# Kernel tuning notes

Hardware: AMD Instinct MI355X
Metric: run time of the kernel (lower is better)

The kernel has to match this reference:

```python
import jax, jax.numpy as jnp
import numpy as np

B, S, D = 2, 2048, 1024
H, KVH, HD = 16, 4, 64          # query heads, kv heads, head dim
E, TOPK, F = 8, 2, 4096          # experts, top-k, expert intermediate
BAL_COEF = 0.01
EPS = 1e-6
ROPE_THETA = 10000.0


def setup_inputs() -> dict:
    key = jax.random.key(0)
    ks = jax.random.split(key, 10)
    g = lambda k, shape, sc=0.02: jax.random.normal(k, shape, dtype=jnp.float32) * sc
    return {
        "hidden_states": jax.random.normal(ks[0], (B, S, D), dtype=jnp.float32),
        "ln1_w": jnp.ones((D,), jnp.float32),
        "wq": g(ks[1], (D, H * HD)),
        "wk": g(ks[2], (D, KVH * HD)),
        "wv": g(ks[3], (D, KVH * HD)),
        "wo": g(ks[4], (H * HD, D)),
        "ln2_w": jnp.ones((D,), jnp.float32),
        "router_w": g(ks[5], (E, D)),
        "w_gate": g(ks[6], (E, D, F)),
        "w_up": g(ks[7], (E, D, F)),
        "w_down": g(ks[8], (E, F, D)),
    }


def rmsnorm(x, w):
    var = jnp.mean(jnp.square(x), axis=-1, keepdims=True)
    return x * jax.lax.rsqrt(var + EPS) * w


def apply_rope(x, pos):
    # x: [B, S, h, d]; HF rotate-half convention
    d = x.shape[-1]
    inv_freq = 1.0 / (ROPE_THETA ** (jnp.arange(0, d, 2, dtype=jnp.float32) / d))
    ang = pos.astype(jnp.float32)[:, None] * inv_freq[None, :]        # [S, d/2]
    cos = jnp.cos(ang)[None, :, None, :]
    sin = jnp.sin(ang)[None, :, None, :]
    x1, x2 = jnp.split(x, 2, axis=-1)
    return jnp.concatenate([x1 * cos - x2 * sin, x2 * cos + x1 * sin], axis=-1)


def reference(hidden_states, ln1_w, wq, wk, wv, wo, ln2_w, router_w, w_gate, w_up, w_down):
    b, s, d = hidden_states.shape
    pos = jnp.arange(s)

    # ---- RMSNorm -> GQA -> residual ----
    h = rmsnorm(hidden_states, ln1_w)
    q = (h @ wq).reshape(b, s, H, HD)
    k = (h @ wk).reshape(b, s, KVH, HD)
    v = (h @ wv).reshape(b, s, KVH, HD)
    q = apply_rope(q, pos)
    k = apply_rope(k, pos)
    rep = H // KVH
    k = jnp.repeat(k, rep, axis=2)   # [B,S,H,HD]
    v = jnp.repeat(v, rep, axis=2)

    scores = jnp.einsum("bshd,bthd->bhst", q, k) * (HD ** -0.5)
    causal = jnp.tril(jnp.ones((s, s), dtype=bool))
    scores = jnp.where(causal[None, None], scores, jnp.finfo(scores.dtype).min)
    attn = jax.nn.softmax(scores, axis=-1)
    ctx = jnp.einsum("bhst,bthd->bshd", attn, v).reshape(b, s, H * HD)
    hidden_states = hidden_states + ctx @ wo

    # ---- RMSNorm -> MoE -> residual ----
    h2 = rmsnorm(hidden_states, ln2_w)
    x = h2.reshape(-1, d)                                    # [T, D]
    logits = x @ router_w.T                                  # [T, E]
    probs = jax.nn.softmax(logits, axis=-1)
    top_p, top_i = jax.lax.top_k(probs, TOPK)                # [T, K]
    top_p = top_p / jnp.sum(top_p, axis=-1, keepdims=True)   # renormalize
    gates = jnp.zeros_like(probs).at[jnp.arange(x.shape[0])[:, None], top_i].set(top_p)  # [T, E]

    moe_out = jnp.zeros_like(x)
    for e in range(E):  # fixed small expert count
        gate = jax.nn.silu(x @ w_gate[e]) * (x @ w_up[e])    # SwiGLU [T, F]
        moe_out = moe_out + gates[:, e:e + 1] * (gate @ w_down[e])

    # ---- load-balancing aux loss (Switch-style) ----
    sel = jnp.sum(jax.nn.one_hot(top_i, E, dtype=probs.dtype), axis=1)  # [T, E]
    frac = jnp.mean(sel, axis=0) / TOPK                       # fraction routed, sums to 1
    prob_mean = jnp.mean(probs, axis=0)
    balance_loss = BAL_COEF * E * jnp.sum(frac * prob_mean)

    out = hidden_states + moe_out.reshape(b, s, d)
    return out, balance_loss
```

## Files before the change

kernel.cpp:

```cpp
#include <hip/hip_runtime.h>

#define Tt 4096
#define Bb 2
#define Ss 2048
#define Dd 1024
#define Hh 16
#define KVHn 4
#define HDn 64
#define En 8
#define Fn 4096

#define BM 128
#define BN 128

typedef unsigned short u16;
typedef __attribute__((ext_vector_type(4))) float f32x4;
typedef __attribute__((ext_vector_type(8))) short bfrag;
typedef __attribute__((ext_vector_type(4))) short s16x4;

#define WAITV(N) asm volatile("s_waitcnt vmcnt(" #N ")" ::: "memory")
#define BARRIER() asm volatile("s_barrier" ::: "memory")

__device__ __forceinline__ u16 f2bf(float f) {
    unsigned u = __builtin_bit_cast(unsigned, f);
    u = (u + 0x7fffu + ((u >> 16) & 1u)) >> 16;
    return (u16)u;
}
__device__ __forceinline__ float bf2f(u16 b) {
    unsigned u = ((unsigned)b) << 16;
    return __builtin_bit_cast(float, u);
}
__device__ __forceinline__ void split8a(const float* va, bfrag* ph, bfrag* pl) {
    bfrag th, tl;
#pragma unroll
    for (int j = 0; j < 8; j++) {
        u16 hu = f2bf(va[j]);
        th[j] = (short)hu;
        tl[j] = (short)f2bf(va[j] - bf2f(hu));
    }
    *ph = th; *pl = tl;
}
__device__ __forceinline__ void glds16(const void* g, void* l) {
    __builtin_amdgcn_global_load_lds(
        (const __attribute__((address_space(1))) unsigned int*)g,
        (__attribute__((address_space(3))) unsigned int*)l, 16, 0, 0);
}

template<bool SPL>
__global__ __launch_bounds__(256)
void tconv_k(const float* __restrict__ src, u16* __restrict__ dhi, u16* __restrict__ dlo,
             const int K, const int N, const int rowOff, const int nTilesN)
{
    const int tid = threadIdx.x;
    const int ty = blockIdx.x / nTilesN, tx = blockIdx.x % nTilesN;
    const int k0 = ty * 64, n0 = tx * 64;
    __shared__ float tl[64][65];
#pragma unroll
    for (int it = 0; it < 16; it++) {
        int idx = tid + it * 256;
        int kk = idx >> 6, nn = idx & 63;
        tl[kk][nn] = src[(size_t)(k0 + kk) * N + n0 + nn];
    }
    __syncthreads();
#pragma unroll
    for (int it = 0; it < 8; it++) {
        int idx = tid + it * 256;
        int n = idx >> 5, k2 = (idx & 31) * 2;
        float v0 = tl[k2][n], v1 = tl[k2 + 1][n];
        u16 h0 = f2bf(v0), h1v = f2bf(v1);
        size_t o = (size_t)(rowOff + n0 + n) * K + k0 + k2;
        *(unsigned*)&dhi[o] = (unsigned)h0 | ((unsigned)h1v << 16);
        if (SPL) {
            u16 l0 = f2bf(v0 - bf2f(h0)), l1 = f2bf(v1 - bf2f(h1v));
            *(unsigned*)&dlo[o] = (unsigned)l0 | ((unsigned)l1 << 16);
        }
    }
}

template<int TBK, bool SWZ>
__global__ __launch_bounds__(256)
void tprep_k(const float* __restrict__ src, u16* __restrict__ dst,
             const int K, const int N, const int nTilesN)
{
    const int tid = threadIdx.x;
    const int e = blockIdx.y;
    const int ntl = blockIdx.x % nTilesN, kt = blockIdx.x / nTilesN;
    const int nTK = K / TBK;
    src += (size_t)e * K * N + (size_t)(kt * TBK) * N + ntl * 128;
    u16* dblk = dst + (((size_t)e * nTilesN + ntl) * nTK + kt) * (size_t)(128 * TBK);
    __shared__ float tl[TBK][132];
#pragma unroll
    for (int it = 0; it < TBK / 8; it++) {
        int i4 = tid + it * 256;
        int kk = i4 >> 5, n = (i4 & 31) * 4;
        f32x4 v = *(const f32x4*)(src + (size_t)kk * N + n);
        tl[kk][n] = v.x; tl[kk][n + 1] = v.y; tl[kk][n + 2] = v.z; tl[kk][n + 3] = v.w;
    }
    __syncthreads();
#pragma unroll
    for (int it = 0; it < TBK / 16; it++) {
        int idx = tid + it * 256;
        int n = (TBK == 32) ? (idx >> 2) : (idx >> 3);
        int c = (TBK == 32) ? (idx & 3) : (idx & 7);
        bfrag v;
#pragma unroll
        for (int j = 0; j < 8; j++) v[j] = (short)f2bf(tl[c * 8 + j][n]);
        int boff = n * (TBK * 2) + ((c * 16) ^ (SWZ ? ((n & 7) << 4) : 0));
        *(bfrag*)((char*)dblk + boff) = v;
    }
}

__global__ __launch_bounds__(256)
void rmsnorm_split_k(const float* __restrict__ x, const float* __restrict__ w,
                     u16* __restrict__ ohi, u16* __restrict__ olo)
{
    const int row = blockIdx.x;
    const int tid = threadIdx.x;
    const int lane = tid & 63, wid = tid >> 6;
    f32x4 t4 = *(const f32x4*)(x + (size_t)row * Dd + tid * 4);
    float s = t4.x*t4.x + t4.y*t4.y + t4.z*t4.z + t4.w*t4.w;
#pragma unroll
    for (int o = 1; o < 64; o <<= 1) s += __shfl_xor(s, o, 64);
    __shared__ float red[4];
    if (lane == 0) red[wid] = s;
    __syncthreads();
    float inv = rsqrtf((red[0] + red[1] + red[2] + red[3]) * (1.0f / Dd) + 1e-6f);
    f32x4 w4 = *(const f32x4*)(w + tid * 4);
    float va[4] = { t4.x*inv*w4.x, t4.y*inv*w4.y, t4.z*inv*w4.z, t4.w*inv*w4.w };
    s16x4 hi, lo;
#pragma unroll
    for (int j = 0; j < 4; j++) {
        u16 hu = f2bf(va[j]);
        hi[j] = (short)hu;
        lo[j] = (short)f2bf(va[j] - bf2f(hu));
    }
    *(s16x4*)&ohi[(size_t)row * Dd + tid * 4] = hi;
    *(s16x4*)&olo[(size_t)row * Dd + tid * 4] = lo;
}

__global__ __launch_bounds__(256)
void rmsnorm2_k(const float* __restrict__ x, const float* __restrict__ w,
                float* __restrict__ of, u16* __restrict__ ob)
{
    const int row = blockIdx.x;
    const int tid = threadIdx.x;
    const int lane = tid & 63, wid = tid >> 6;
    f32x4 t4 = *(const f32x4*)(x + (size_t)row * Dd + tid * 4);
    float s = t4.x*t4.x + t4.y*t4.y + t4.z*t4.z + t4.w*t4.w;
#pragma unroll
    for (int o = 1; o < 64; o <<= 1) s += __shfl_xor(s, o, 64);
    __shared__ float red[4];
    if (lane == 0) red[wid] = s;
    __syncthreads();
    float inv = rsqrtf((red[0] + red[1] + red[2] + red[3]) * (1.0f / Dd) + 1e-6f);
    f32x4 w4 = *(const f32x4*)(w + tid * 4);
    f32x4 o4;
    o4.x = t4.x*inv*w4.x; o4.y = t4.y*inv*w4.y; o4.z = t4.z*inv*w4.z; o4.w = t4.w*inv*w4.w;
    *(f32x4*)&of[(size_t)row * Dd + tid * 4] = o4;
    s16x4 hb;
    hb[0] = (short)f2bf(o4.x); hb[1] = (short)f2bf(o4.y);
    hb[2] = (short)f2bf(o4.z); hb[3] = (short)f2bf(o4.w);
    *(s16x4*)&ob[(size_t)row * Dd + tid * 4] = hb;
}

__global__ __launch_bounds__(256)
void rope_tab_k(float* __restrict__ ct, float* __restrict__ st)
{
    int idx = blockIdx.x * 256 + threadIdx.x;
    if (idx < Ss * 32) {
        int s = idx >> 5, i = idx & 31;
        double inv = pow(10000.0, -((double)(2 * i)) / 64.0);
        double a = (double)s * inv;
        double sn, cs;
        sincos(a, &sn, &cs);
        ct[idx] = (float)cs;
        st[idx] = (float)sn;
    }
}

__global__ __launch_bounds__(256)
void rope_q_k(float* __restrict__ qkv, const float* __restrict__ ct, const float* __restrict__ st)
{
    int idx = blockIdx.x * 256 + threadIdx.x;
    int i = idx & 31, hh = (idx >> 5) & (Hh - 1), t = idx >> 9;
    int s = t & (Ss - 1);
    float cs = ct[s * 32 + i], sn = st[s * 32 + i];
    float* base = qkv + (size_t)t * 1536 + hh * 64 + i;
    float x1 = base[0], x2 = base[32];
    base[0]  = x1 * cs - x2 * sn;
    base[32] = x2 * cs + x1 * sn;
}

__global__ __launch_bounds__(256)
void kprep_k(const float* __restrict__ qkv, const float* __restrict__ ct,
             const float* __restrict__ st, u16* __restrict__ khi, u16* __restrict__ klo)
{
    int idx = blockIdx.x * 256 + threadIdx.x;
    int i = idx & 31, hh = (idx >> 5) & (KVHn - 1), t = idx >> 7;
    int s = t & (Ss - 1);
    float cs = ct[s * 32 + i], sn = st[s * 32 + i];
    const float* base = qkv + (size_t)t * 1536 + 1024 + hh * 64 + i;
    float x1 = base[0], x2 = base[32];
    float r1 = x1 * cs - x2 * sn, r2 = x2 * cs + x1 * sn;
    size_t o = (size_t)t * (KVHn * HDn) + hh * 64 + i;
    u16 h1v = f2bf(r1), h2v = f2bf(r2);
    khi[o] = h1v;       khi[o + 32] = h2v;
    klo[o] = f2bf(r1 - bf2f(h1v));
    klo[o + 32] = f2bf(r2 - bf2f(h2v));
}

__global__ __launch_bounds__(256)
void vprep_k(const float* __restrict__ qkv, u16* __restrict__ vthi, u16* __restrict__ vtlo)
{
    const int st0 = blockIdx.x * 64;
    const int g = blockIdx.y;
    const int b = g >> 2, kvh = g & 3;
    const int tid = threadIdx.x;
    __shared__ float tl[64][65];
#pragma unroll
    for (int it = 0; it < 16; it++) {
        int idx = tid + it * 256;
        int sl = idx >> 6, d = idx & 63;
        tl[sl][d] = qkv[(size_t)(b * Ss + st0 + sl) * 1536 + 1280 + kvh * 64 + d];
    }
    __syncthreads();
#pragma unroll
    for (int it = 0; it < 8; it++) {
        int idx = tid + it * 256;
        int d = idx >> 5, s2 = (idx & 31) * 2;
        float v0 = tl[s2][d], v1 = tl[s2 + 1][d];
        u16 h0 = f2bf(v0), h1v = f2bf(v1);
        size_t o = ((size_t)g * 64 + d) * Ss + st0 + s2;
        *(unsigned*)&vthi[o] = (unsigned)h0 | ((unsigned)h1v << 16);
        u16 l0 = f2bf(v0 - bf2f(h0)), l1 = f2bf(v1 - bf2f(h1v));
        *(unsigned*)&vtlo[o] = (unsigned)l0 | ((unsigned)l1 << 16);
    }
}

template<bool RESID>
__global__ __launch_bounds__(256)
void gemm_split_k(const u16* __restrict__ Ahi_g, const u16* __restrict__ Alo_g,
                  const u16* __restrict__ Bhi_g, const u16* __restrict__ Blo_g,
                  float* __restrict__ C, const float* __restrict__ resid,
                  const int M, const int N, const int K, const int ntiles)
{
    const int bid = blockIdx.x;
    const int nt = bid % ntiles, mt = bid / ntiles;
    __shared__ __align__(16) u16 Ah[2][128 * 32], Al[2][128 * 32];
    __shared__ __align__(16) u16 Bh[2][128 * 32], Bl[2][128 * 32];
    const int tid = threadIdx.x, lane = tid & 63, wid = tid >> 6;
    const int wrow = (wid >> 1) * 64, wcol = (wid & 1) * 64;
    const int l15 = lane & 15, lhi = lane >> 4;
    const int row0 = mt * BM, col0 = nt * BN;

    const u16 *ah_s[2], *al_s[2], *bh_s[2], *bl_s[2];
#pragma unroll
    for (int j = 0; j < 2; j++) {
        int r = (wid * 2 + j) * 16 + (lane >> 2);
        size_t ca = (size_t)(row0 + r) * K + (lane & 3) * 8;
        size_t cb = (size_t)(col0 + r) * K + (lane & 3) * 8;
        ah_s[j] = Ahi_g + ca; al_s[j] = Alo_g + ca;
        bh_s[j] = Bhi_g + cb; bl_s[j] = Blo_g + cb;
    }
    f32x4 acc[4][4];
#pragma unroll
    for (int i = 0; i < 4; i++)
#pragma unroll
        for (int j = 0; j < 4; j++) { acc[i][j].x = 0.f; acc[i][j].y = 0.f; acc[i][j].z = 0.f; acc[i][j].w = 0.f; }

    auto stage = [&](int buf, int k0) {
#pragma unroll
        for (int j = 0; j < 2; j++) {
            int d = (wid * 2 + j) * 512;
            glds16(ah_s[j] + k0, &Ah[buf][d]);
            glds16(al_s[j] + k0, &Al[buf][d]);
            glds16(bh_s[j] + k0, &Bh[buf][d]);
            glds16(bl_s[j] + k0, &Bl[buf][d]);
        }
    };
    auto compute = [&](int cur) {
        bfrag ah[4], al[4], bh[4], bl[4];
#pragma unroll
        for (int mi = 0; mi < 4; mi++) {
            int rb = (wrow + mi * 16 + l15) * 32 + lhi * 8;
            ah[mi] = *(const bfrag*)&Ah[cur][rb];
            al[mi] = *(const bfrag*)&Al[cur][rb];
        }
#pragma unroll
        for (int ni = 0; ni < 4; ni++) {
            int rb = (wcol + ni * 16 + l15) * 32 + lhi * 8;
            bh[ni] = *(const bfrag*)&Bh[cur][rb];
            bl[ni] = *(const bfrag*)&Bl[cur][rb];
        }
#pragma unroll
        for (int mi = 0; mi < 4; mi++)
#pragma unroll
            for (int ni = 0; ni < 4; ni++) {
                acc[mi][ni] = __builtin_amdgcn_mfma_f32_16x16x32_bf16(ah[mi], bh[ni], acc[mi][ni], 0, 0, 0);
                acc[mi][ni] = __builtin_amdgcn_mfma_f32_16x16x32_bf16(ah[mi], bl[ni], acc[mi][ni], 0, 0, 0);
                acc[mi][ni] = __builtin_amdgcn_mfma_f32_16x16x32_bf16(al[mi], bh[ni], acc[mi][ni], 0, 0, 0);
            }
    };
    const int nkt = K / 32;
    stage(0, 0);
    stage(1, 32);
    int cur = 0;
    for (int kt = 0; kt < nkt - 1; kt++) {
        WAITV(8);
        BARRIER();
        compute(cur);
        BARRIER();
        if (kt + 2 < nkt) stage(cur, (kt + 2) * 32);
        cur ^= 1;
    }
    WAITV(0);
    BARRIER();
    compute(cur);
#pragma unroll
    for (int mi = 0; mi < 4; mi++) {
#pragma unroll
        for (int t = 0; t < 4; t++) {
            int pr = row0 + wrow + mi * 16 + lhi * 4 + t;
#pragma unroll
            for (int ni = 0; ni < 4; ni++) {
                int gc = col0 + wcol + ni * 16 + l15;
                float vv = acc[mi][ni][t];
                if (RESID) vv += resid[(size_t)pr * N + gc];
                C[(size_t)pr * N + gc] = vv;
            }
        }
    }
}

template<int MODE>
__global__ __launch_bounds__(256, 4)
void gemm_expert_k(const u16* __restrict__ A_g, const u16* __restrict__ Bt,
                   u16* __restrict__ act,
                   const int* __restrict__ toklist, const float* __restrict__ gwlist,
                   const int* __restrict__ counts, const int* __restrict__ offsets)
{
    const int e = blockIdx.y;
    const int Meff = counts[e];
    const int nt = blockIdx.x & 31, mt = blockIdx.x >> 5;
    if (mt * BM >= Meff) return;
    const int* tok = toklist + e * Tt;
    const float* gw = gwlist + e * Tt;
    const int rowoff = offsets[e];
    __shared__ __align__(16) u16 As[2][128 * 32], Bs[2][128 * 32];
    const int tid = threadIdx.x, lane = tid & 63, wid = tid >> 6;
    const int wrow = (wid >> 1) * 64, wcol = (wid & 1) * 64;
    const int l15 = lane & 15, lhi = lane >> 4;
    const int row0 = mt * BM, col0 = nt * BN;

    const u16* asrc[2];
#pragma unroll
    for (int j = 0; j < 2; j++) {
        int row = (wid * 2 + j) * 16 + (lane >> 2);
        int pr = row0 + row;
        int tr = (pr < Meff) ? tok[pr] : tok[0];
        asrc[j] = A_g + (size_t)tr * Dd + (lane & 3) * 8;
    }
    const size_t bblk = (size_t)(e * 32 + nt) * (32 * 4096);
    const u16* bsrc = Bt + bblk + (size_t)(wid * 2) * 512 + lane * 8;

    f32x4 acc[4][4];
#pragma unroll
    for (int i = 0; i < 4; i++)
#pragma unroll
        for (int j = 0; j < 4; j++) { acc[i][j].x = 0.f; acc[i][j].y = 0.f; acc[i][j].z = 0.f; acc[i][j].w = 0.f; }

    auto stage = [&](int buf, int kt) {
#pragma unroll
        for (int j = 0; j < 2; j++) {
            int d = (wid * 2 + j) * 512;
            glds16(asrc[j] + kt * 32,                  &As[buf][d]);
            glds16(bsrc + j * 512 + (size_t)kt * 4096, &Bs[buf][d]);
        }
    };
    auto compute = [&](int cur) {
        bfrag a[4];
#pragma unroll
        for (int mi = 0; mi < 4; mi++)
            a[mi] = *(const bfrag*)&As[cur][(wrow + mi * 16 + l15) * 32 + lhi * 8];
#pragma unroll
        for (int ni = 0; ni < 4; ni++) {
            bfrag b = *(const bfrag*)&Bs[cur][(wcol + ni * 16 + l15) * 32 + lhi * 8];
#pragma unroll
            for (int mi = 0; mi < 4; mi++)
                acc[mi][ni] = __builtin_amdgcn_mfma_f32_16x16x32_bf16(a[mi], b, acc[mi][ni], 0, 0, 0);
        }
    };
    stage(0, 0);
    stage(1, 1);
    int cur = 0;
    for (int kt = 0; kt < 31; kt++) {
        WAITV(4);
        BARRIER();
        compute(cur);
        BARRIER();
        if (kt + 2 < 32) stage(cur, kt + 2);
        cur ^= 1;
    }
    WAITV(0);
    BARRIER();
    compute(cur);
#pragma unroll
    for (int mi = 0; mi < 4; mi++) {
#pragma unroll
        for (int t = 0; t < 4; t++) {
            int pr = row0 + wrow + mi * 16 + lhi * 4 + t;
            if (pr < Meff) {
                float gwv = (MODE == 1) ? gw[pr] : 0.f;
#pragma unroll
                for (int ni = 0; ni < 4; ni++) {
                    int gc = col0 + wcol + ni * 16 + l15;
                    size_t ix = (size_t)(rowoff + pr) * Fn + gc;
                    if (MODE == 0) {
                        act[ix] = f2bf(acc[mi][ni][t]);
                    } else {
                        float g = bf2f(act[ix]);
                        float sg = g / (1.0f + expf(-g));
                        act[ix] = f2bf(sg * acc[mi][ni][t] * gwv);
                    }
                }
            }
        }
    }
}

__global__ __launch_bounds__(256, 4)
void gemm_down_k(const u16* __restrict__ act, const u16* __restrict__ Bt,
                 float* __restrict__ C, const int* __restrict__ toklist,
                 const int* __restrict__ counts, const int* __restrict__ offsets)
{
    const int e = blockIdx.y;
    const int Meff = counts[e];
    const int nt = blockIdx.x & 7, mt = blockIdx.x >> 3;
    if (mt * BM >= Meff) return;
    const int* tok = toklist + e * Tt;
    const int rowoff = offsets[e];
    __shared__ __align__(16) u16 As[2][128 * 32], Bs[2][128 * 32];
    const int tid = threadIdx.x, lane = tid & 63, wid = tid >> 6;
    const int wrow = (wid >> 1) * 64, wcol = (wid & 1) * 64;
    const int l15 = lane & 15, lhi = lane >> 4;
    const int row0 = mt * BM;

    const u16* asrc[2];
#pragma unroll
    for (int j = 0; j < 2; j++) {
        int row = (wid * 2 + j) * 16 + (lane >> 2);
        int pr = row0 + row;
        int rr = (pr < Meff) ? pr : 0;
        asrc[j] = act + (size_t)(rowoff + rr) * Fn + (lane & 3) * 8;
    }
    const size_t bblk = (size_t)(e * 8 + nt) * ((size_t)128 * 4096);
    const u16* bsrc = Bt + bblk + (size_t)(wid * 2) * 512 + lane * 8;

    f32x4 acc[4][4];
#pragma unroll
    for (int i = 0; i < 4; i++)
#pragma unroll
        for (int j = 0; j < 4; j++) { acc[i][j].x = 0.f; acc[i][j].y = 0.f; acc[i][j].z = 0.f; acc[i][j].w = 0.f; }

    auto stage = [&](int buf, int kt) {
#pragma unroll
        for (int j = 0; j < 2; j++) {
            int d = (wid * 2 + j) * 512;
            glds16(asrc[j] + kt * 32,                  &As[buf][d]);
            glds16(bsrc + j * 512 + (size_t)kt * 4096, &Bs[buf][d]);
        }
    };
    auto compute = [&](int cur) {
        bfrag a[4];
#pragma unroll
        for (int mi = 0; mi < 4; mi++)
            a[mi] = *(const bfrag*)&As[cur][(wrow + mi * 16 + l15) * 32 + lhi * 8];
#pragma unroll
        for (int ni = 0; ni < 4; ni++) {
            bfrag b = *(const bfrag*)&Bs[cur][(wcol + ni * 16 + l15) * 32 + lhi * 8];
#pragma unroll
            for (int mi = 0; mi < 4; mi++)
                acc[mi][ni] = __builtin_amdgcn_mfma_f32_16x16x32_bf16(a[mi], b, acc[mi][ni], 0, 0, 0);
        }
    };
    stage(0, 0);
    stage(1, 1);
    int cur = 0;
    const int nkt = Fn / 32;
    for (int kt = 0; kt < nkt - 1; kt++) {
        WAITV(4);
        BARRIER();
        compute(cur);
        BARRIER();
        if (kt + 2 < nkt) stage(cur, kt + 2);
        cur ^= 1;
    }
    WAITV(0);
    BARRIER();
    compute(cur);
#pragma unroll
    for (int mi = 0; mi < 4; mi++) {
#pragma unroll
        for (int t = 0; t < 4; t++) {
            int pr = row0 + wrow + mi * 16 + lhi * 4 + t;
            if (pr < Meff) {
                int trow = tok[pr];
#pragma unroll
                for (int ni = 0; ni < 4; ni++) {
                    int gc = nt * BN + wcol + ni * 16 + l15;
                    atomicAdd(&C[(size_t)trow * Dd + gc], acc[mi][ni][t]);
                }
            }
        }
    }
}

__global__ __launch_bounds__(256)
void attn_k(const float* __restrict__ qkv, const u16* __restrict__ khi,
            const u16* __restrict__ klo, const u16* __restrict__ vthi,
            const u16* __restrict__ vtlo, u16* __restrict__ chi, u16* __restrict__ clo)
{
    const int qt = (int)gridDim.x - 1 - (int)blockIdx.x;
    const int h = blockIdx.y, b = blockIdx.z;
    const int kvh = h >> 2;
    const int g = b * KVHn + kvh;
    const int tid = threadIdx.x;
    const int lane = tid & 63, wid = tid >> 6;
    const int l15 = lane & 15, lhi = lane >> 4;

    __shared__ __align__(16) u16 Khi[64 * 64];
    __shared__ __align__(16) u16 Klo[64 * 64];
    __shared__ __align__(16) u16 Vhi[64 * 72];
    __shared__ __align__(16) u16 Vlo[64 * 72];
    __shared__ __align__(16) u16 Phi[4 * 16 * 72];
    __shared__ __align__(16) u16 Plo[4 * 16 * 72];

    bfrag qh[2], ql[2];
    {
        const int qrow = qt * 64 + wid * 16 + l15;
        const float* qb = qkv + (size_t)(b * Ss + qrow) * 1536 + h * 64;
#pragma unroll
        for (int ks = 0; ks < 2; ks++) {
            const float* p = qb + ks * 32 + lhi * 8;
            f32x4 u0 = *(const f32x4*)p;
            f32x4 u1 = *(const f32x4*)(p + 4);
            float va[8] = { u0.x * 0.125f, u0.y * 0.125f, u0.z * 0.125f, u0.w * 0.125f,
                            u1.x * 0.125f, u1.y * 0.125f, u1.z * 0.125f, u1.w * 0.125f };
            split8a(va, &qh[ks], &ql[ks]);
        }
    }
    size_t kga[2], vga[2];
    int kboff[2], vboff[2];
#pragma unroll
    for (int it = 0; it < 2; it++) {
        int ci = tid + it * 256;
        int kv = ci >> 3, d0 = (ci & 7) << 3;
        kga[it] = (size_t)(b * Ss + kv) * (KVHn * HDn) + kvh * 64 + d0;
        kboff[it] = kv * 128 + ((d0 * 2) ^ ((kv & 7) << 4));
        int d = ci >> 3, kv0 = (ci & 7) << 3;
        vga[it] = ((size_t)g * 64 + d) * Ss + kv0;
        vboff[it] = d * 72 + kv0;
    }
    bfrag rkh[2], rkl[2], rvh[2], rvl[2];
    auto LOADR = [&](int kt) {
#pragma unroll
        for (int it = 0; it < 2; it++) {
            size_t ga = kga[it] + (size_t)kt * (64 * KVHn * HDn);
            rkh[it] = *(const bfrag*)&khi[ga];
            rkl[it] = *(const bfrag*)&klo[ga];
            size_t gv = vga[it] + (size_t)kt * 64;
            rvh[it] = *(const bfrag*)&vthi[gv];
            rvl[it] = *(const bfrag*)&vtlo[gv];
        }
    };
    f32x4 O[4];
#pragma unroll
    for (int ni = 0; ni < 4; ni++) { O[ni].x = 0.f; O[ni].y = 0.f; O[ni].z = 0.f; O[ni].w = 0.f; }
    float m_s = -1e30f;
    float l_s = 0.f;

    LOADR(0);
    for (int kt = 0; kt <= qt; kt++) {
#pragma unroll
        for (int it = 0; it < 2; it++) {
            *(bfrag*)((char*)Khi + kboff[it]) = rkh[it];
            *(bfrag*)((char*)Klo + kboff[it]) = rkl[it];
            *(bfrag*)&Vhi[vboff[it]] = rvh[it];
            *(bfrag*)&Vlo[vboff[it]] = rvl[it];
        }
        __syncthreads();
        if (kt < qt) LOADR(kt + 1);
        f32x4 sf[4];
#pragma unroll
        for (int ni = 0; ni < 4; ni++) { sf[ni].x = 0.f; sf[ni].y = 0.f; sf[ni].z = 0.f; sf[ni].w = 0.f; }
        __builtin_amdgcn_s_setprio(1);
#pragma unroll
        for (int ks = 0; ks < 2; ks++) {
#pragma unroll
            for (int ni = 0; ni < 4; ni++) {
                int kv = ni * 16 + l15;
                int dof = ks * 64 + lhi * 16;
                int boff = kv * 128 + (dof ^ ((kv & 7) << 4));
                bfrag kfh = *(const bfrag*)((const char*)Khi + boff);
                bfrag kfl = *(const bfrag*)((const char*)Klo + boff);
                sf[ni] = __builtin_amdgcn_mfma_f32_16x16x32_bf16(kfh, qh[ks], sf[ni], 0, 0, 0);
                sf[ni] = __builtin_amdgcn_mfma_f32_16x16x32_bf16(kfl, qh[ks], sf[ni], 0, 0, 0);
                sf[ni] = __builtin_amdgcn_mfma_f32_16x16x32_bf16(kfh, ql[ks], sf[ni], 0, 0, 0);
            }
        }
        __builtin_amdgcn_s_setprio(0);
        if (kt == qt) {
#pragma unroll
            for (int ni = 0; ni < 4; ni++)
#pragma unroll
                for (int t = 0; t < 4; t++)
                    if (ni * 16 + lhi * 4 + t > wid * 16 + l15) sf[ni][t] = -1e30f;
        }
        float mx = -1e30f;
#pragma unroll
        for (int ni = 0; ni < 4; ni++)
#pragma unroll
            for (int t = 0; t < 4; t++) mx = fmaxf(mx, sf[ni][t]);
        mx = fmaxf(mx, __shfl_xor(mx, 16, 64));
        mx = fmaxf(mx, __shfl_xor(mx, 32, 64));
        float mn = fmaxf(m_s, mx);
        float sc = expf(m_s - mn);
        m_s = mn;
        float rs = 0.f;
#pragma unroll
        for (int ni = 0; ni < 4; ni++)
#pragma unroll
            for (int t = 0; t < 4; t++) {
                float p = expf(sf[ni][t] - mn);
                sf[ni][t] = p;
                rs += p;
            }
        rs += __shfl_xor(rs, 16, 64);
        rs += __shfl_xor(rs, 32, 64);
        l_s = l_s * sc + rs;
#pragma unroll
        for (int ni = 0; ni < 4; ni++)
#pragma unroll
            for (int t = 0; t < 4; t++) O[ni][t] *= sc;
#pragma unroll
        for (int ni = 0; ni < 4; ni++)
#pragma unroll
            for (int t = 0; t < 4; t++) {
                float p = sf[ni][t];
                u16 hu = f2bf(p);
                int ix = (wid * 16 + l15) * 72 + ni * 16 + lhi * 4 + t;
                Phi[ix] = hu;
                Plo[ix] = f2bf(p - bf2f(hu));
            }
        asm volatile("s_waitcnt lgkmcnt(0)" ::: "memory");
        __builtin_amdgcn_sched_barrier(0);
        __builtin_amdgcn_s_setprio(1);
#pragma unroll
        for (int ks = 0; ks < 2; ks++) {
            int pb = (wid * 16 + l15) * 72 + ks * 32 + lhi * 8;
            bfrag pfh = *(const bfrag*)&Phi[pb];
            bfrag pfl = *(const bfrag*)&Plo[pb];
#pragma unroll
            for (int ni = 0; ni < 4; ni++) {
                int vb = (ni * 16 + l15) * 72 + ks * 32 + lhi * 8;
                bfrag vfh = *(const bfrag*)&Vhi[vb];
                bfrag vfl = *(const bfrag*)&Vlo[vb];
                O[ni] = __builtin_amdgcn_mfma_f32_16x16x32_bf16(vfh, pfh, O[ni], 0, 0, 0);
                O[ni] = __builtin_amdgcn_mfma_f32_16x16x32_bf16(vfl, pfh, O[ni], 0, 0, 0);
                O[ni] = __builtin_amdgcn_mfma_f32_16x16x32_bf16(vfh, pfl, O[ni], 0, 0, 0);
            }
        }
        __builtin_amdgcn_s_setprio(0);
        __syncthreads();
    }
    {
        float inv = 1.0f / l_s;
        int qrow = qt * 64 + wid * 16 + l15;
        size_t base = (size_t)(b * Ss + qrow) * Dd + h * 64;
#pragma unroll
        for (int ni = 0; ni < 4; ni++)
#pragma unroll
            for (int t = 0; t < 4; t++) {
                float val = O[ni][t] * inv;
                u16 hv = f2bf(val);
                int d = ni * 16 + lhi * 4 + t;
                chi[base + d] = hv;
                clo[base + d] = f2bf(val - bf2f(hv));
            }
    }
}

__global__ __launch_bounds__(256)
void router_k(const float* __restrict__ h2, const float* __restrict__ rw,
              float* __restrict__ probs, int* __restrict__ counts,
              int* __restrict__ toklist, float* __restrict__ gwlist)
{
    const int t = blockIdx.x;
    const int tid = threadIdx.x;
    const int lane = tid & 63, wid = tid >> 6;
    f32x4 x4 = *(const f32x4*)(h2 + (size_t)t * Dd + tid * 4);
    float part[En];
#pragma unroll
    for (int e = 0; e < En; e++) {
        f32x4 w4 = *(const f32x4*)(rw + (size_t)e * Dd + tid * 4);
        part[e] = x4.x * w4.x + x4.y * w4.y + x4.z * w4.z + x4.w * w4.w;
    }
#pragma unroll
    for (int e = 0; e < En; e++)
#pragma unroll
        for (int o = 1; o < 64; o <<= 1) part[e] += __shfl_xor(part[e], o, 64);
    __shared__ float red[4][En];
    if (lane == 0) {
#pragma unroll
        for (int e = 0; e < En; e++) red[wid][e] = part[e];
    }
    __syncthreads();
    if (tid == 0) {
        float lg[En];
        float mx = -1e30f;
#pragma unroll
        for (int e = 0; e < En; e++) {
            lg[e] = red[0][e] + red[1][e] + red[2][e] + red[3][e];
            mx = fmaxf(mx, lg[e]);
        }
        float pe[En], ssum = 0.f;
#pragma unroll
        for (int e = 0; e < En; e++) { pe[e] = expf(lg[e] - mx); ssum += pe[e]; }
        float inv = 1.0f / ssum;
#pragma unroll
        for (int e = 0; e < En; e++) { pe[e] *= inv; probs[(size_t)t * En + e] = pe[e]; }
        int i0 = 0;
#pragma unroll
        for (int e = 1; e < En; e++) if (pe[e] > pe[i0]) i0 = e;
        int i1 = (i0 == 0) ? 1 : 0;
#pragma unroll
        for (int e = 0; e < En; e++) if (e != i0 && pe[e] > pe[i1]) i1 = e;
        float s2 = pe[i0] + pe[i1];
        int s0 = atomicAdd(&counts[i0], 1);
        toklist[i0 * Tt + s0] = t; gwlist[i0 * Tt + s0] = pe[i0] / s2;
        int s1 = atomicAdd(&counts[i1], 1);
        toklist[i1 * Tt + s1] = t; gwlist[i1 * Tt + s1] = pe[i1] / s2;
    }
}

__global__ __launch_bounds__(256)
void finalize_k(const float* __restrict__ probs, const int* __restrict__ counts,
                int* __restrict__ offsets, float* __restrict__ loss_out)
{
    const int tid = threadIdx.x, lane = tid & 63, wid = tid >> 6;
    float ps[En];
#pragma unroll
    for (int e = 0; e < En; e++) ps[e] = 0.f;
    for (int t = tid; t < Tt; t += 256) {
#pragma unroll
        for (int e = 0; e < En; e++) ps[e] += probs[(size_t)t * En + e];
    }
#pragma unroll
    for (int e = 0; e < En; e++)
#pragma unroll
        for (int o = 1; o < 64; o <<= 1) ps[e] += __shfl_xor(ps[e], o, 64);
    __shared__ float red[4][En];
    if (lane == 0) {
#pragma unroll
        for (int e = 0; e < En; e++) red[wid][e] = ps[e];
    }
    __syncthreads();
    if (tid == 0) {
        int o = 0;
        float bl = 0.f;
#pragma unroll
        for (int e = 0; e < En; e++) {
            offsets[e] = o; o += counts[e];
            float pm = (red[0][e] + red[1][e] + red[2][e] + red[3][e]) * (1.0f / Tt);
            float fr = (float)counts[e] * (1.0f / (Tt * 2));
            bl += fr * pm;
        }
        loss_out[0] = 0.01f * (float)En * bl;
    }
}

extern "C" void kernel_launch(void* const* d_in, const int* in_sizes, int n_in,
                              void* d_out, int out_size, void* d_ws, size_t ws_size,
                              hipStream_t stream)
{
    (void)in_sizes; (void)n_in; (void)out_size; (void)ws_size;
    const float* hs  = (const float*)d_in[0];
    const float* ln1 = (const float*)d_in[1];
    const float* wq  = (const float*)d_in[2];
    const float* wk  = (const float*)d_in[3];
    const float* wv  = (const float*)d_in[4];
    const float* wo  = (const float*)d_in[5];
    const float* ln2 = (const float*)d_in[6];
    const float* rw  = (const float*)d_in[7];
    const float* wg  = (const float*)d_in[8];
    const float* wu  = (const float*)d_in[9];
    const float* wd  = (const float*)d_in[10];
    float* out = (float*)d_out;

    char* ws = (char*)d_ws;
    size_t off = 0;
    auto nxt = [&](size_t bytes) { char* p = ws + off; off += (bytes + 255) & ~(size_t)255; return p; };
    u16* wgt  = (u16*)nxt((size_t)En * Fn * Dd * 2);
    u16* wut  = (u16*)nxt((size_t)En * Fn * Dd * 2);
    u16* wdt  = (u16*)nxt((size_t)En * Dd * Fn * 2);
    float* h2 = (float*)nxt((size_t)Tt * Dd * 4);
    u16* h2b  = (u16*)nxt((size_t)Tt * Dd * 2);
    float* probs = (float*)nxt((size_t)Tt * En * 4);
    int*   tokl  = (int*)nxt((size_t)En * Tt * 4);
    float* gwl   = (float*)nxt((size_t)En * Tt * 4);
    float* ctab  = (float*)nxt((size_t)Ss * 32 * 4);
    float* stab  = (float*)nxt((size_t)Ss * 32 * 4);
    int* counts  = (int*)nxt(256);
    int* offs    = (int*)nxt(256);
    u16* act = (u16*)(ws + off);
    float* qkv = (float*)nxt((size_t)Tt * 1536 * 4);
    u16* h1hi = (u16*)nxt((size_t)Tt * Dd * 2);
    u16* h1lo = (u16*)nxt((size_t)Tt * Dd * 2);
    u16* khi  = (u16*)nxt((size_t)Tt * KVHn * HDn * 2);
    u16* klo  = (u16*)nxt((size_t)Tt * KVHn * HDn * 2);
    u16* vthi = (u16*)nxt((size_t)Tt * KVHn * HDn * 2);
    u16* vtlo = (u16*)nxt((size_t)Tt * KVHn * HDn * 2);
    u16* chi  = (u16*)nxt((size_t)Tt * Dd * 2);
    u16* clo  = (u16*)nxt((size_t)Tt * Dd * 2);
    u16* wqkvthi = (u16*)nxt((size_t)1536 * Dd * 2);
    u16* wqkvtlo = (u16*)nxt((size_t)1536 * Dd * 2);
    u16* wothi = (u16*)nxt((size_t)Dd * Dd * 2);
    u16* wotlo = (u16*)nxt((size_t)Dd * Dd * 2);

    rope_tab_k<<<dim3(256), 256, 0, stream>>>(ctab, stab);
    tconv_k<true ><<<dim3(16 * 16), 256, 0, stream>>>(wq, wqkvthi, wqkvtlo, 1024, 1024,    0, 16);
    tconv_k<true ><<<dim3(16 *  4), 256, 0, stream>>>(wk, wqkvthi, wqkvtlo, 1024,  256, 1024,  4);
    tconv_k<true ><<<dim3(16 *  4), 256, 0, stream>>>(wv, wqkvthi, wqkvtlo, 1024,  256, 1280,  4);
    tconv_k<true ><<<dim3(16 * 16), 256, 0, stream>>>(wo, wothi, wotlo, 1024, 1024, 0, 16);
    tprep_k<32, false><<<dim3(32 * 32, En), 256, 0, stream>>>(wg, wgt, 1024, 4096, 32);
    tprep_k<32, false><<<dim3(32 * 32, En), 256, 0, stream>>>(wu, wut, 1024, 4096, 32);
    tprep_k<32, false><<<dim3(8 * 128, En), 256, 0, stream>>>(wd, wdt, 4096, 1024, 8);

    rmsnorm_split_k<<<dim3(Tt), 256, 0, stream>>>(hs, ln1, h1hi, h1lo);
    gemm_split_k<false><<<dim3(12 * 32), 256, 0, stream>>>(h1hi, h1lo, wqkvthi, wqkvtlo,
                                                           qkv, nullptr, Tt, 1536, Dd, 12);
    rope_q_k<<<dim3(Tt * Hh * 32 / 256), 256, 0, stream>>>(qkv, ctab, stab);
    kprep_k<<<dim3(Tt * KVHn * 32 / 256), 256, 0, stream>>>(qkv, ctab, stab, khi, klo);
    vprep_k<<<dim3(Ss / 64, Bb * KVHn), 256, 0, stream>>>(qkv, vthi, vtlo);
    attn_k<<<dim3(Ss / 64, Hh, Bb), 256, 0, stream>>>(qkv, khi, klo, vthi, vtlo, chi, clo);
    gemm_split_k<true><<<dim3(8 * 32), 256, 0, stream>>>(chi, clo, wothi, wotlo,
                                                         out, hs, Tt, Dd, Dd, 8);
    rmsnorm2_k<<<dim3(Tt), 256, 0, stream>>>(out, ln2, h2, h2b);
    (void)hipMemsetAsync(counts, 0, 64, stream);
    router_k<<<dim3(Tt), 256, 0, stream>>>(h2, rw, probs, counts, tokl, gwl);
    finalize_k<<<dim3(1), 256, 0, stream>>>(probs, counts, offs, out + (size_t)Tt * Dd);
    gemm_expert_k<0><<<dim3(32 * 32, En), 256, 0, stream>>>(h2b, wgt, act, tokl, gwl, counts, offs);
    gemm_expert_k<1><<<dim3(32 * 32, En), 256, 0, stream>>>(h2b, wut, act, tokl, gwl, counts, offs);
    gemm_down_k<<<dim3(8 * 32, En), 256, 0, stream>>>(act, wdt, out, tokl, counts, offs);
}
```

Measured before the change: 897.7 us.

## Fuse gate and up expert GEMMs into one kernel; lazy softmax rescale in attention

Merges the two expert GEMM launches (gate, then up with a SwiGLU epilogue) into one kernel. The gate result is kept in registers as packed bf16 and the up GEMM runs afterwards in the same block, so the bf16 gate round trip through global memory and one launch go away, at the cost of more registers (launch bounds lowered from 4 to 3). In attention, the online-softmax rescale of O and l is skipped unless the row max grows by more than 8, and P hi/lo stores to LDS are packed into 64-bit writes. The lazy rescale keeps exponentials bounded by e^8, so fp32 accuracy should hold.

```diff
diff --git a/kernel.cpp b/kernel.cpp
--- a/kernel.cpp
+++ b/kernel.cpp
@@ -17,6 +17,7 @@
 typedef __attribute__((ext_vector_type(4))) float f32x4;
 typedef __attribute__((ext_vector_type(8))) short bfrag;
 typedef __attribute__((ext_vector_type(4))) short s16x4;
+typedef __attribute__((ext_vector_type(2))) unsigned u32x2;
 
 #define WAITV(N) asm volatile("s_waitcnt vmcnt(" #N ")" ::: "memory")
 #define BARRIER() asm volatile("s_barrier" ::: "memory")
@@ -332,12 +333,11 @@
     }
 }
 
-template<int MODE>
-__global__ __launch_bounds__(256, 4)
-void gemm_expert_k(const u16* __restrict__ A_g, const u16* __restrict__ Bt,
-                   u16* __restrict__ act,
-                   const int* __restrict__ toklist, const float* __restrict__ gwlist,
-                   const int* __restrict__ counts, const int* __restrict__ offsets)
+__global__ __launch_bounds__(256, 3)
+void gemm_gateup2_k(const u16* __restrict__ A_g, const u16* __restrict__ Gt,
+                    const u16* __restrict__ Ut, u16* __restrict__ act,
+                    const int* __restrict__ toklist, const float* __restrict__ gwlist,
+                    const int* __restrict__ counts, const int* __restrict__ offsets)
 {
     const int e = blockIdx.y;
     const int Meff = counts[e];
@@ -361,7 +361,8 @@
         asrc[j] = A_g + (size_t)tr * Dd + (lane & 3) * 8;
     }
     const size_t bblk = (size_t)(e * 32 + nt) * (32 * 4096);
-    const u16* bsrc = Bt + bblk + (size_t)(wid * 2) * 512 + lane * 8;
+    const u16* gsrc = Gt + bblk + (size_t)(wid * 2) * 512 + lane * 8;
+    const u16* usrc = Ut + bblk + (size_t)(wid * 2) * 512 + lane * 8;
 
     f32x4 acc[4][4];
 #pragma unroll
@@ -369,7 +370,7 @@
 #pragma unroll
         for (int j = 0; j < 4; j++) { acc[i][j].x = 0.f; acc[i][j].y = 0.f; acc[i][j].z = 0.f; acc[i][j].w = 0.f; }
 
-    auto stage = [&](int buf, int kt) {
+    auto stage = [&](int buf, int kt, const u16* bsrc) {
 #pragma unroll
         for (int j = 0; j < 2; j++) {
             int d = (wid * 2 + j) * 512;
@@ -390,38 +391,61 @@
                 acc[mi][ni] = __builtin_amdgcn_mfma_f32_16x16x32_bf16(a[mi], b, acc[mi][ni], 0, 0, 0);
         }
     };
-    stage(0, 0);
-    stage(1, 1);
+    stage(0, 0, gsrc);
+    stage(1, 1, gsrc);
     int cur = 0;
     for (int kt = 0; kt < 31; kt++) {
         WAITV(4);
         BARRIER();
         compute(cur);
         BARRIER();
-        if (kt + 2 < 32) stage(cur, kt + 2);
+        if (kt + 2 < 32) stage(cur, kt + 2, gsrc);
         cur ^= 1;
     }
     WAITV(0);
     BARRIER();
     compute(cur);
+    unsigned garr[32];
+#pragma unroll
+    for (int mi = 0; mi < 4; mi++)
+#pragma unroll
+        for (int ni = 0; ni < 4; ni++) {
+            u16 a0 = f2bf(acc[mi][ni].x), a1 = f2bf(acc[mi][ni].y);
+            u16 a2 = f2bf(acc[mi][ni].z), a3 = f2bf(acc[mi][ni].w);
+            garr[(mi * 4 + ni) * 2 + 0] = (unsigned)a0 | ((unsigned)a1 << 16);
+            garr[(mi * 4 + ni) * 2 + 1] = (unsigned)a2 | ((unsigned)a3 << 16);
+            acc[mi][ni].x = 0.f; acc[mi][ni].y = 0.f; acc[mi][ni].z = 0.f; acc[mi][ni].w = 0.f;
+        }
+    BARRIER();
+    stage(0, 0, usrc);
+    stage(1, 1, usrc);
+    cur = 0;
+    for (int kt = 0; kt < 31; kt++) {
+        WAITV(4);
+        BARRIER();
+        compute(cur);
+        BARRIER();
+        if (kt + 2 < 32) stage(cur, kt + 2, usrc);
+        cur ^= 1;
+    }
+    WAITV(0);
+    BARRIER();
+    compute(cur);
 #pragma unroll
     for (int mi = 0; mi < 4; mi++) {
 #pragma unroll
         for (int t = 0; t < 4; t++) {
             int pr = row0 + wrow + mi * 16 + lhi * 4 + t;
             if (pr < Meff) {
-                float gwv = (MODE == 1) ? gw[pr] : 0.f;
+                float gwv = gw[pr];
 #pragma unroll
                 for (int ni = 0; ni < 4; ni++) {
                     int gc = col0 + wcol + ni * 16 + l15;
                     size_t ix = (size_t)(rowoff + pr) * Fn + gc;
-                    if (MODE == 0) {
-                        act[ix] = f2bf(acc[mi][ni][t]);
-                    } else {
-                        float g = bf2f(act[ix]);
-                        float sg = g / (1.0f + expf(-g));
-                        act[ix] = f2bf(sg * acc[mi][ni][t] * gwv);
-                    }
+                    u16 gu = (u16)(garr[(mi * 4 + ni) * 2 + (t >> 1)] >> ((t & 1) * 16));
+                    float g = bf2f(gu);
+                    float sg = g / (1.0f + expf(-g));
+                    act[ix] = f2bf(sg * acc[mi][ni][t] * gwv);
                 }
             }
         }
@@ -623,35 +647,40 @@
             for (int t = 0; t < 4; t++) mx = fmaxf(mx, sf[ni][t]);
         mx = fmaxf(mx, __shfl_xor(mx, 16, 64));
         mx = fmaxf(mx, __shfl_xor(mx, 32, 64));
-        float mn = fmaxf(m_s, mx);
-        float sc = expf(m_s - mn);
-        m_s = mn;
+        if (!__all(mx <= m_s + 8.0f)) {
+            float mn = fmaxf(m_s, mx);
+            float sc = expf(m_s - mn);
+            m_s = mn;
+#pragma unroll
+            for (int ni = 0; ni < 4; ni++)
+#pragma unroll
+                for (int t = 0; t < 4; t++) O[ni][t] *= sc;
+            l_s *= sc;
+        }
         float rs = 0.f;
 #pragma unroll
         for (int ni = 0; ni < 4; ni++)
 #pragma unroll
             for (int t = 0; t < 4; t++) {
-                float p = expf(sf[ni][t] - mn);
+                float p = expf(sf[ni][t] - m_s);
                 sf[ni][t] = p;
                 rs += p;
             }
         rs += __shfl_xor(rs, 16, 64);
         rs += __shfl_xor(rs, 32, 64);
-        l_s = l_s * sc + rs;
-#pragma unroll
-        for (int ni = 0; ni < 4; ni++)
-#pragma unroll
-            for (int t = 0; t < 4; t++) O[ni][t] *= sc;
-#pragma unroll
-        for (int ni = 0; ni < 4; ni++)
-#pragma unroll
-            for (int t = 0; t < 4; t++) {
-                float p = sf[ni][t];
-                u16 hu = f2bf(p);
-                int ix = (wid * 16 + l15) * 72 + ni * 16 + lhi * 4 + t;
-                Phi[ix] = hu;
-                Plo[ix] = f2bf(p - bf2f(hu));
-            }
+        l_s += rs;
+#pragma unroll
+        for (int ni = 0; ni < 4; ni++) {
+            u16 a0 = f2bf(sf[ni][0]), a1 = f2bf(sf[ni][1]);
+            u16 a2 = f2bf(sf[ni][2]), a3 = f2bf(sf[ni][3]);
+            u16 b0 = f2bf(sf[ni][0] - bf2f(a0)), b1 = f2bf(sf[ni][1] - bf2f(a1));
+            u16 b2 = f2bf(sf[ni][2] - bf2f(a2)), b3 = f2bf(sf[ni][3] - bf2f(a3));
+            int ix = (wid * 16 + l15) * 72 + ni * 16 + lhi * 4;
+            u32x2 hv; hv.x = (unsigned)a0 | ((unsigned)a1 << 16); hv.y = (unsigned)a2 | ((unsigned)a3 << 16);
+            u32x2 lv; lv.x = (unsigned)b0 | ((unsigned)b1 << 16); lv.y = (unsigned)b2 | ((unsigned)b3 << 16);
+            *(u32x2*)&Phi[ix] = hv;
+            *(u32x2*)&Plo[ix] = lv;
+        }
         asm volatile("s_waitcnt lgkmcnt(0)" ::: "memory");
         __builtin_amdgcn_sched_barrier(0);
         __builtin_amdgcn_s_setprio(1);
@@ -849,7 +878,6 @@
     (void)hipMemsetAsync(counts, 0, 64, stream);
     router_k<<<dim3(Tt), 256, 0, stream>>>(h2, rw, probs, counts, tokl, gwl);
     finalize_k<<<dim3(1), 256, 0, stream>>>(probs, counts, offs, out + (size_t)Tt * Dd);
-    gemm_expert_k<0><<<dim3(32 * 32, En), 256, 0, stream>>>(h2b, wgt, act, tokl, gwl, counts, offs);
-    gemm_expert_k<1><<<dim3(32 * 32, En), 256, 0, stream>>>(h2b, wut, act, tokl, gwl, counts, offs);
+    gemm_gateup2_k<<<dim3(32 * 32, En), 256, 0, stream>>>(h2b, wgt, wut, act, tokl, gwl, counts, offs);
     gemm_down_k<<<dim3(8 * 32, En), 256, 0, stream>>>(act, wdt, out, tokl, counts, offs);
 }
```

Result: slower. 923.5 us (+2.9%).

## Read K and V fragments directly from global memory in attention kernel

Applied to the files above, without the earlier changes.

Removes the shared-memory staging of K and V tiles, along with the register prefetch and the block-wide barriers, from the attention kernel. Each wave now loads its MFMA fragments straight from global (cache-backed) memory. This saves LDS traffic and synchronisation, but each of the four waves re-reads the same K/V tile from global memory, and the loads are no longer prefetched ahead of compute, so load latency is exposed. Some unused placeholder code (kbase) is left behind.

```diff
diff --git a/kernel.cpp b/kernel.cpp
--- a/kernel.cpp
+++ b/kernel.cpp
@@ -528,10 +528,6 @@
     const int lane = tid & 63, wid = tid >> 6;
     const int l15 = lane & 15, lhi = lane >> 4;
 
-    __shared__ __align__(16) u16 Khi[64 * 64];
-    __shared__ __align__(16) u16 Klo[64 * 64];
-    __shared__ __align__(16) u16 Vhi[64 * 72];
-    __shared__ __align__(16) u16 Vlo[64 * 72];
     __shared__ __align__(16) u16 Phi[4 * 16 * 72];
     __shared__ __align__(16) u16 Plo[4 * 16 * 72];
 
@@ -549,47 +545,15 @@
             split8a(va, &qh[ks], &ql[ks]);
         }
     }
-    size_t kga[2], vga[2];
-    int kboff[2], vboff[2];
-#pragma unroll
-    for (int it = 0; it < 2; it++) {
-        int ci = tid + it * 256;
-        int kv = ci >> 3, d0 = (ci & 7) << 3;
-        kga[it] = (size_t)(b * Ss + kv) * (KVHn * HDn) + kvh * 64 + d0;
-        kboff[it] = kv * 128 + ((d0 * 2) ^ ((kv & 7) << 4));
-        int d = ci >> 3, kv0 = (ci & 7) << 3;
-        vga[it] = ((size_t)g * 64 + d) * Ss + kv0;
-        vboff[it] = d * 72 + kv0;
-    }
-    bfrag rkh[2], rkl[2], rvh[2], rvl[2];
-    auto LOADR = [&](int kt) {
-#pragma unroll
-        for (int it = 0; it < 2; it++) {
-            size_t ga = kga[it] + (size_t)kt * (64 * KVHn * HDn);
-            rkh[it] = *(const bfrag*)&khi[ga];
-            rkl[it] = *(const bfrag*)&klo[ga];
-            size_t gv = vga[it] + (size_t)kt * 64;
-            rvh[it] = *(const bfrag*)&vthi[gv];
-            rvl[it] = *(const bfrag*)&vtlo[gv];
-        }
-    };
+    const u16* kbase = khi;
     f32x4 O[4];
 #pragma unroll
     for (int ni = 0; ni < 4; ni++) { O[ni].x = 0.f; O[ni].y = 0.f; O[ni].z = 0.f; O[ni].w = 0.f; }
     float m_s = -1e30f;
     float l_s = 0.f;
-
-    LOADR(0);
+    (void)kbase;
+
     for (int kt = 0; kt <= qt; kt++) {
-#pragma unroll
-        for (int it = 0; it < 2; it++) {
-            *(bfrag*)((char*)Khi + kboff[it]) = rkh[it];
-            *(bfrag*)((char*)Klo + kboff[it]) = rkl[it];
-            *(bfrag*)&Vhi[vboff[it]] = rvh[it];
-            *(bfrag*)&Vlo[vboff[it]] = rvl[it];
-        }
-        __syncthreads();
-        if (kt < qt) LOADR(kt + 1);
         f32x4 sf[4];
 #pragma unroll
         for (int ni = 0; ni < 4; ni++) { sf[ni].x = 0.f; sf[ni].y = 0.f; sf[ni].z = 0.f; sf[ni].w = 0.f; }
@@ -599,10 +563,9 @@
 #pragma unroll
             for (int ni = 0; ni < 4; ni++) {
                 int kv = ni * 16 + l15;
-                int dof = ks * 64 + lhi * 16;
-                int boff = kv * 128 + (dof ^ ((kv & 7) << 4));
-                bfrag kfh = *(const bfrag*)((const char*)Khi + boff);
-                bfrag kfl = *(const bfrag*)((const char*)Klo + boff);
+                size_t ka = (size_t)(b * Ss + kt * 64 + kv) * (KVHn * HDn) + kvh * 64 + ks * 32 + lhi * 8;
+                bfrag kfh = *(const bfrag*)&khi[ka];
+                bfrag kfl = *(const bfrag*)&klo[ka];
                 sf[ni] = __builtin_amdgcn_mfma_f32_16x16x32_bf16(kfh, qh[ks], sf[ni], 0, 0, 0);
                 sf[ni] = __builtin_amdgcn_mfma_f32_16x16x32_bf16(kfl, qh[ks], sf[ni], 0, 0, 0);
                 sf[ni] = __builtin_amdgcn_mfma_f32_16x16x32_bf16(kfh, ql[ks], sf[ni], 0, 0, 0);
@@ -662,16 +625,16 @@
             bfrag pfl = *(const bfrag*)&Plo[pb];
 #pragma unroll
             for (int ni = 0; ni < 4; ni++) {
-                int vb = (ni * 16 + l15) * 72 + ks * 32 + lhi * 8;
-                bfrag vfh = *(const bfrag*)&Vhi[vb];
-                bfrag vfl = *(const bfrag*)&Vlo[vb];
+                int d = ni * 16 + l15;
+                size_t va = ((size_t)g * 64 + d) * Ss + kt * 64 + ks * 32 + lhi * 8;
+                bfrag vfh = *(const bfrag*)&vthi[va];
+                bfrag vfl = *(const bfrag*)&vtlo[va];
                 O[ni] = __builtin_amdgcn_mfma_f32_16x16x32_bf16(vfh, pfh, O[ni], 0, 0, 0);
                 O[ni] = __builtin_amdgcn_mfma_f32_16x16x32_bf16(vfl, pfh, O[ni], 0, 0, 0);
                 O[ni] = __builtin_amdgcn_mfma_f32_16x16x32_bf16(vfh, pfl, O[ni], 0, 0, 0);
             }
         }
         __builtin_amdgcn_s_setprio(0);
-        __syncthreads();
     }
     {
         float inv = 1.0f / l_s;
```

Result: slower. 1.180 ms (+31.5%).
